# Kernel optimization log

Measured on AMD Instinct MI355X. Metric: run time of the kernel, lower is better.

Reference implementation:

```python
import jax, jax.numpy as jnp
import numpy as np

LN_EPS = 1e-5  # nn.LayerNorm default
N_HEAD = 12


def layer_norm(x, w, b, eps=LN_EPS):
    m = jnp.mean(x, axis=-1, keepdims=True)
    v = jnp.var(x, axis=-1, keepdims=True)
    return (x - m) * jax.lax.rsqrt(v + eps) * w + b


def mha(x, in_proj_w, in_proj_b, out_w, out_b, n_head):
    # x: [B,S,D]; self-attention, q=k=v=x (torch nn.MultiheadAttention math)
    B, S, D = x.shape
    hd = D // n_head
    qkv = x @ in_proj_w.T + in_proj_b              # [B,S,3D]
    q, k, v = jnp.split(qkv, 3, axis=-1)
    q = q.reshape(B, S, n_head, hd)
    k = k.reshape(B, S, n_head, hd)
    v = v.reshape(B, S, n_head, hd)
    scale = 1.0 / jnp.sqrt(jnp.asarray(hd, x.dtype))
    scores = jnp.einsum('bqhd,bkhd->bhqk', q, k) * scale  # [B,H,S,S]
    attn = jax.nn.softmax(scores, axis=-1)
    o = jnp.einsum('bhqk,bkhd->bqhd', attn, v).reshape(B, S, D)
    return o @ out_w.T + out_b


def setup_inputs() -> dict:
    key = jax.random.key(0)
    ks = jax.random.split(key, 8)
    B, S, D = 4, 2048, 768
    d_ff = 4 * D
    sd = 0.02
    return {
        'x': jax.random.normal(ks[0], (B, S, D), jnp.float32),
        'ln1_w': jnp.ones((D,), jnp.float32),
        'ln1_b': jnp.zeros((D,), jnp.float32),
        'in_proj_w': jax.random.normal(ks[1], (3 * D, D), jnp.float32) * sd,
        'in_proj_b': jax.random.normal(ks[2], (3 * D,), jnp.float32) * sd,
        'out_w': jax.random.normal(ks[3], (D, D), jnp.float32) * sd,
        'out_b': jax.random.normal(ks[4], (D,), jnp.float32) * sd,
        'ln2_w': jnp.ones((D,), jnp.float32),
        'ln2_b': jnp.zeros((D,), jnp.float32),
        'fc_w': jax.random.normal(ks[5], (d_ff, D), jnp.float32) * sd,
        'fc_b': jnp.zeros((d_ff,), jnp.float32),
        'proj_w': jax.random.normal(ks[6], (D, d_ff), jnp.float32) * sd,
        'proj_b': jnp.zeros((D,), jnp.float32),
    }


def reference(x, ln1_w, ln1_b, in_proj_w, in_proj_b, out_w, out_b,
              ln2_w, ln2_b, fc_w, fc_b, proj_w, proj_b):
    h = layer_norm(x, ln1_w, ln1_b)
    x = x + mha(h, in_proj_w, in_proj_b, out_w, out_b, N_HEAD)
    h2 = layer_norm(x, ln2_w, ln2_b)
    mlp = jax.nn.gelu(h2 @ fc_w.T + fc_b, approximate=False) @ proj_w.T + proj_b
    return x + mlp
```

## Files before the change

### kernel.cpp

```cpp
#include <hip/hip_runtime.h>
#include <hip/hip_bf16.h>
#include <math.h>

#define D_MODEL 768
#define N_HEADS 12
#define HD 64
#define SEQ 2048
#define BATCH 4
#define M_ROWS 8192
#define D_FF 3072
#define QKV_DIM 2304
#define LN_EPS 1e-5f
#define Q_SCALE 0.18033688011112042f

typedef __attribute__((ext_vector_type(8))) short bf16x8;
typedef __attribute__((ext_vector_type(4))) float f32x4;
typedef __hip_bfloat16 bf16;

__device__ __forceinline__ void store_val(float* p, float v) { *p = v; }
__device__ __forceinline__ void store_val(bf16* p, float v) { *p = __float2bfloat16(v); }

__device__ __forceinline__ unsigned int pack_bf16_pair(float a, float b) {
    unsigned int ua = __builtin_bit_cast(unsigned int, a) + 0x8000u;
    unsigned int ub = __builtin_bit_cast(unsigned int, b) + 0x8000u;
    return __builtin_amdgcn_perm(ub, ua, 0x07060302u);
}

__device__ __forceinline__ void async_load16(const void* g, void* l) {
    __builtin_amdgcn_global_load_lds(
        (const __attribute__((address_space(1))) void*)g,
        (__attribute__((address_space(3))) void*)l, 16, 0, 0);
}

__global__ __launch_bounds__(256) void ln1_cast(
        const float* __restrict__ x, const float* __restrict__ w,
        const float* __restrict__ b, bf16* __restrict__ y,
        const float* __restrict__ s0, bf16* __restrict__ d0, int n0,
        const float* __restrict__ s1, bf16* __restrict__ d1, int n1,
        const float* __restrict__ s2, bf16* __restrict__ d2, int n2,
        const float* __restrict__ s3, bf16* __restrict__ d3, int n3) {
    int t = threadIdx.x;
    if (blockIdx.x >= M_ROWS) {
        int i = (blockIdx.x - M_ROWS) * 256 + t;
        const float* s; bf16* d; int local = i;
        if (local < n0) { s = s0; d = d0; }
        else {
            local -= n0;
            if (local < n1) { s = s1; d = d1; }
            else {
                local -= n1;
                if (local < n2) { s = s2; d = d2; }
                else {
                    local -= n2;
                    if (local >= n3) return;
                    s = s3; d = d3;
                }
            }
        }
        float4 v = ((const float4*)s)[local];
        uint2 pk;
        pk.x = pack_bf16_pair(v.x, v.y);
        pk.y = pack_bf16_pair(v.z, v.w);
        *(uint2*)(d + local * 4) = pk;
        return;
    }
    int row = blockIdx.x;
    const float* xr = x + (size_t)row * D_MODEL;
    bf16* yr = y + (size_t)row * D_MODEL;
    float v0 = xr[t], v1 = xr[t + 256], v2 = xr[t + 512];
    float s  = v0 + v1 + v2;
    float sq = v0 * v0 + v1 * v1 + v2 * v2;
    #pragma unroll
    for (int off = 32; off; off >>= 1) {
        s  += __shfl_xor(s, off);
        sq += __shfl_xor(sq, off);
    }
    __shared__ float ss[4], ssq[4];
    int wave = t >> 6;
    if ((t & 63) == 0) { ss[wave] = s; ssq[wave] = sq; }
    __syncthreads();
    s  = ss[0] + ss[1] + ss[2] + ss[3];
    sq = ssq[0] + ssq[1] + ssq[2] + ssq[3];
    float mean = s * (1.0f / D_MODEL);
    float var  = sq * (1.0f / D_MODEL) - mean * mean;
    float rstd = rsqrtf(var + LN_EPS);
    yr[t]       = __float2bfloat16((v0 - mean) * rstd * w[t]       + b[t]);
    yr[t + 256] = __float2bfloat16((v1 - mean) * rstd * w[t + 256] + b[t + 256]);
    yr[t + 512] = __float2bfloat16((v2 - mean) * rstd * w[t + 512] + b[t + 512]);
}

template <typename OutT>
__global__ __launch_bounds__(256) void ln_kernel(const float* __restrict__ x,
                                                 const float* __restrict__ w,
                                                 const float* __restrict__ b,
                                                 OutT* __restrict__ y) {
    int row = blockIdx.x;
    const float* xr = x + (size_t)row * D_MODEL;
    OutT* yr = y + (size_t)row * D_MODEL;
    int t = threadIdx.x;
    float v0 = xr[t], v1 = xr[t + 256], v2 = xr[t + 512];
    float s  = v0 + v1 + v2;
    float sq = v0 * v0 + v1 * v1 + v2 * v2;
    #pragma unroll
    for (int off = 32; off; off >>= 1) {
        s  += __shfl_xor(s, off);
        sq += __shfl_xor(sq, off);
    }
    __shared__ float ss[4], ssq[4];
    int wave = t >> 6;
    if ((t & 63) == 0) { ss[wave] = s; ssq[wave] = sq; }
    __syncthreads();
    s  = ss[0] + ss[1] + ss[2] + ss[3];
    sq = ssq[0] + ssq[1] + ssq[2] + ssq[3];
    float mean = s * (1.0f / D_MODEL);
    float var  = sq * (1.0f / D_MODEL) - mean * mean;
    float rstd = rsqrtf(var + LN_EPS);
    store_val(yr + t,       (v0 - mean) * rstd * w[t]       + b[t]);
    store_val(yr + t + 256, (v1 - mean) * rstd * w[t + 256] + b[t + 256]);
    store_val(yr + t + 512, (v2 - mean) * rstd * w[t + 512] + b[t + 512]);
}

__device__ __forceinline__ float gelu_fast(float v) {
    float u = v * (0.7978845608f + 0.0356774081f * v * v);
    u = fminf(fmaxf(u, -10.0f), 10.0f);
    float e = __builtin_amdgcn_exp2f(u * 2.8853900818f);
    float th = (e - 1.0f) * __builtin_amdgcn_rcpf(e + 1.0f);
    return 0.5f * v * (1.0f + th);
}

template <int FUSE, typename OutT>
__global__ __launch_bounds__(256) void gemm_mfma(const bf16* __restrict__ A,
                                                 const bf16* __restrict__ W,
                                                 const float* __restrict__ bias,
                                                 const float* __restrict__ resid,
                                                 OutT* __restrict__ C,
                                                 int M, int N, int K) {
    const int BK = 64;
    __shared__ __align__(16) bf16 As[2][128 * BK];
    __shared__ __align__(16) bf16 Bs[2][128 * BK];
    int t = threadIdx.x;
    int wave = t >> 6, lane = t & 63;

    int nbx = gridDim.x;
    int w0 = blockIdx.x + nbx * blockIdx.y;
    int cpx = (nbx * gridDim.y) >> 3;
    int wg = (w0 & 7) * cpx + (w0 >> 3);
    int m_base = (wg / nbx) * 128, n_base = (wg % nbx) * 128;

    int wm = (wave >> 1) * 64, wn = (wave & 1) * 64;
    int c = lane & 15, rr = lane >> 4;
    int cx = c & 7;

    f32x4 acc[4][4] = {};

    const bf16* Ag[4]; const bf16* Bg[4];
    int loff[4];
    #pragma unroll
    for (int r = 0; r < 4; r++) {
        int s = r * 256 + t;
        int row = s >> 3, p = s & 7;
        int kc = p ^ (row & 7);
        Ag[r] = A + (size_t)(m_base + row) * K + kc * 8;
        Bg[r] = W + (size_t)(n_base + row) * K + kc * 8;
        loff[r] = (r * 256 + wave * 64) * 8;
    }

    auto STAGE = [&](int kt, int buf) {
        int k0 = kt * BK;
        #pragma unroll
        for (int r = 0; r < 4; r++) {
            async_load16(Ag[r] + k0, As[buf] + loff[r]);
            async_load16(Bg[r] + k0, Bs[buf] + loff[r]);
        }
    };

    int nk = K / BK;
    STAGE(0, 0);
    STAGE(1, 1);

    for (int ki = 0; ki < nk; ki++) {
        int cur = ki & 1;
        if (ki < nk - 1) {
            asm volatile("s_waitcnt vmcnt(8)" ::: "memory");
        } else {
            asm volatile("s_waitcnt vmcnt(0)" ::: "memory");
        }
        __builtin_amdgcn_s_barrier();
        __builtin_amdgcn_sched_barrier(0);

        bf16x8 af[2][4], bfr[2][4];
        #pragma unroll
        for (int kk = 0; kk < 2; kk++) {
            int sw = ((kk * 4 + rr) ^ cx) * 8;
            #pragma unroll
            for (int mi = 0; mi < 4; mi++)
                af[kk][mi] = *(const bf16x8*)&As[cur][(wm + mi * 16 + c) * BK + sw];
            #pragma unroll
            for (int ni = 0; ni < 4; ni++)
                bfr[kk][ni] = *(const bf16x8*)&Bs[cur][(wn + ni * 16 + c) * BK + sw];
        }
        asm volatile("s_waitcnt lgkmcnt(0)" ::: "memory");
        __builtin_amdgcn_s_barrier();
        __builtin_amdgcn_sched_barrier(0);

        if (ki + 2 < nk) STAGE(ki + 2, cur);

        __builtin_amdgcn_s_setprio(1);
        #pragma unroll
        for (int kk = 0; kk < 2; kk++)
            #pragma unroll
            for (int mi = 0; mi < 4; mi++)
                #pragma unroll
                for (int ni = 0; ni < 4; ni++)
                    acc[mi][ni] = __builtin_amdgcn_mfma_f32_16x16x32_bf16(
                        bfr[kk][ni], af[kk][mi], acc[mi][ni], 0, 0, 0);
        __builtin_amdgcn_s_setprio(0);
    }

    #pragma unroll
    for (int mi = 0; mi < 4; mi++) {
        int m = m_base + wm + mi * 16 + c;
        #pragma unroll
        for (int ni = 0; ni < 4; ni++) {
            int n0 = n_base + wn + ni * 16 + rr * 4;
            float4 bv = *(const float4*)&bias[n0];
            float v0 = acc[mi][ni][0] + bv.x;
            float v1 = acc[mi][ni][1] + bv.y;
            float v2 = acc[mi][ni][2] + bv.z;
            float v3 = acc[mi][ni][3] + bv.w;
            if (FUSE == 1) {
                v0 = gelu_fast(v0); v1 = gelu_fast(v1);
                v2 = gelu_fast(v2); v3 = gelu_fast(v3);
            }
            if (FUSE == 2) {
                float4 rv = *(const float4*)&resid[(size_t)m * N + n0];
                v0 += rv.x; v1 += rv.y; v2 += rv.z; v3 += rv.w;
            }
            if (FUSE == 3 && n0 < 768) {
                v0 *= Q_SCALE; v1 *= Q_SCALE; v2 *= Q_SCALE; v3 *= Q_SCALE;
            }
            OutT* dst = C + (size_t)m * N + n0;
            if (sizeof(OutT) == 4) {
                float4 st = {v0, v1, v2, v3};
                *(float4*)dst = st;
            } else {
                uint2 pk;
                pk.x = pack_bf16_pair(v0, v1);
                pk.y = pack_bf16_pair(v2, v3);
                *(uint2*)dst = pk;
            }
        }
    }
}

__global__ __launch_bounds__(256) void vtrans(const bf16* __restrict__ qkvb,
                                              bf16* __restrict__ vt) {
    __shared__ bf16 T[64 * 72];
    int t = threadIdx.x;
    int s0 = blockIdx.x * 64, h = blockIdx.y, b = blockIdx.z;
    const bf16* src = qkvb + (size_t)(b * SEQ) * QKV_DIM + 2 * D_MODEL + h * HD;
    #pragma unroll
    for (int i = 0; i < 2; i++) {
        int idx = i * 256 + t;
        int sr = idx >> 3, ch = idx & 7;
        uint4 v = *(const uint4*)(src + (size_t)(s0 + sr) * QKV_DIM + ch * 8);
        *(uint4*)&T[sr * 72 + ch * 8] = v;
    }
    __syncthreads();
    int dr = t >> 2, part = t & 3;
    unsigned int w[8];
    #pragma unroll
    for (int i = 0; i < 8; i++) {
        unsigned short a, bsh;
        __builtin_memcpy(&a,   &T[(part * 16 + 2 * i    ) * 72 + dr], 2);
        __builtin_memcpy(&bsh, &T[(part * 16 + 2 * i + 1) * 72 + dr], 2);
        w[i] = (unsigned int)a | ((unsigned int)bsh << 16);
    }
    bf16* dst = vt + ((size_t)((b * N_HEADS + h) * HD + dr)) * SEQ + s0 + part * 16;
    uint4 p0; p0.x = w[0]; p0.y = w[1]; p0.z = w[2]; p0.w = w[3];
    uint4 p1; p1.x = w[4]; p1.y = w[5]; p1.z = w[6]; p1.w = w[7];
    *(uint4*)dst = p0;
    *(uint4*)(dst + 8) = p1;
}

__global__ __launch_bounds__(256) void attn_mfma(const bf16* __restrict__ qkvb,
                                                 const bf16* __restrict__ vt,
                                                 bf16* __restrict__ o) {
    __shared__ __align__(16) bf16 Ks[2 * 64 * 64];
    __shared__ __align__(16) bf16 Vts[2 * 64 * 64];
    __shared__ __align__(16) bf16 Ps[128 * 64];

    int t = threadIdx.x;
    int wave = t >> 6, lane = t & 63;

    int w0 = blockIdx.x + 16 * (blockIdx.y + 12 * blockIdx.z);
    int wg = (w0 & 7) * 96 + (w0 >> 3);
    int qt = wg & 15;
    int hb = wg >> 4;
    int h = hb % 12, b = hb / 12;

    int s0 = qt * 128;
    int wq = wave * 32;
    int c = lane & 15, rr = lane >> 4;
    int cx = c & 7;

    const bf16* qbase  = qkvb + (size_t)b * SEQ * QKV_DIM + h * HD;
    const bf16* kbase  = qbase + D_MODEL;
    const bf16* vtbase = vt + (size_t)((b * N_HEADS + h) * HD) * SEQ;

    #pragma unroll
    for (int r = 0; r < 4; r++) {
        int lin = r * 256 + t;
        int qq = lin >> 3, p = lin & 7;
        int kc = p ^ (qq & 7);
        async_load16(qbase + (size_t)(s0 + qq) * QKV_DIM + kc * 8,
                     Ps + (size_t)(r * 256 + wave * 64) * 8);
    }
    #pragma unroll
    for (int r = 0; r < 2; r++) {
        int row = (r * 256 + t) >> 3;
        int kc = ((r * 256 + t) & 7) ^ (row & 7);
        async_load16(kbase + (size_t)row * QKV_DIM + kc * 8,
                     Ks + (size_t)(r * 256 + wave * 64) * 8);
        async_load16(vtbase + (size_t)row * SEQ + kc * 8,
                     Vts + (size_t)(r * 256 + wave * 64) * 8);
    }
    __syncthreads();

    bf16x8 bq[2][2];
    #pragma unroll
    for (int m = 0; m < 2; m++)
        #pragma unroll
        for (int kk = 0; kk < 2; kk++)
            bq[m][kk] = *(const bf16x8*)&Ps[(wq + m * 16 + c) * 64 + ((kk * 4 + rr) ^ cx) * 8];

    bf16x8 ones;
    #pragma unroll
    for (int i = 0; i < 8; i++) ones[i] = (short)0x3F80;

    f32x4 Oa[2][4] = {};
    f32x4 La[2] = {};

    for (int jt = 0; jt < SEQ; jt += 64) {
        int cur = (jt >> 6) & 1;
        bf16* Kb  = Ks  + cur * 4096;
        bf16* Vtb = Vts + cur * 4096;

        if (jt + 64 < SEQ) {
            bf16* Kn  = Ks  + (cur ^ 1) * 4096;
            bf16* Vtn = Vts + (cur ^ 1) * 4096;
            #pragma unroll
            for (int r = 0; r < 2; r++) {
                int row = (r * 256 + t) >> 3;
                int kc = ((r * 256 + t) & 7) ^ (row & 7);
                async_load16(kbase + (size_t)(jt + 64 + row) * QKV_DIM + kc * 8,
                             Kn + (size_t)(r * 256 + wave * 64) * 8);
                async_load16(vtbase + (size_t)row * SEQ + (jt + 64) + kc * 8,
                             Vtn + (size_t)(r * 256 + wave * 64) * 8);
            }
        }

        f32x4 St[4][2] = {};
        __builtin_amdgcn_s_setprio(1);
        #pragma unroll
        for (int kk = 0; kk < 2; kk++) {
            bf16x8 ak[4];
            #pragma unroll
            for (int jj = 0; jj < 4; jj++)
                ak[jj] = *(const bf16x8*)&Kb[(jj * 16 + c) * 64 + ((kk * 4 + rr) ^ cx) * 8];
            #pragma unroll
            for (int jj = 0; jj < 4; jj++)
                #pragma unroll
                for (int m = 0; m < 2; m++)
                    St[jj][m] = __builtin_amdgcn_mfma_f32_16x16x32_bf16(
                        ak[jj], bq[m][kk], St[jj][m], 0, 0, 0);
        }
        __builtin_amdgcn_s_setprio(0);

        #pragma unroll
        for (int jj = 0; jj < 4; jj++) {
            int off = ((jj * 2 + (rr >> 1)) ^ cx) * 8 + (rr & 1) * 4;
            #pragma unroll
            for (int m = 0; m < 2; m++) {
                float p0 = __builtin_amdgcn_exp2f(St[jj][m][0]);
                float p1 = __builtin_amdgcn_exp2f(St[jj][m][1]);
                float p2 = __builtin_amdgcn_exp2f(St[jj][m][2]);
                float p3 = __builtin_amdgcn_exp2f(St[jj][m][3]);
                uint2 pk;
                pk.x = pack_bf16_pair(p0, p1);
                pk.y = pack_bf16_pair(p2, p3);
                *(uint2*)&Ps[(wq + m * 16 + c) * 64 + off] = pk;
            }
        }

        __builtin_amdgcn_s_setprio(1);
        #pragma unroll
        for (int kk = 0; kk < 2; kk++) {
            bf16x8 ap[2];
            #pragma unroll
            for (int m = 0; m < 2; m++)
                ap[m] = *(const bf16x8*)&Ps[(wq + m * 16 + c) * 64 + ((kk * 4 + rr) ^ cx) * 8];
            #pragma unroll
            for (int m = 0; m < 2; m++)
                La[m] = __builtin_amdgcn_mfma_f32_16x16x32_bf16(
                    ap[m], ones, La[m], 0, 0, 0);
            #pragma unroll
            for (int n = 0; n < 4; n++) {
                bf16x8 bv = *(const bf16x8*)&Vtb[(n * 16 + c) * 64 + ((kk * 4 + rr) ^ cx) * 8];
                #pragma unroll
                for (int m = 0; m < 2; m++)
                    Oa[m][n] = __builtin_amdgcn_mfma_f32_16x16x32_bf16(
                        ap[m], bv, Oa[m][n], 0, 0, 0);
            }
        }
        __builtin_amdgcn_s_setprio(0);

        __syncthreads();
    }

    #pragma unroll
    for (int m = 0; m < 2; m++)
        #pragma unroll
        for (int rg = 0; rg < 4; rg++) {
            float inv = __builtin_amdgcn_rcpf(La[m][rg]);
            int q = s0 + wq + m * 16 + rr * 4 + rg;
            bf16* op = o + (size_t)(b * SEQ + q) * D_MODEL + h * HD;
            #pragma unroll
            for (int n = 0; n < 4; n++)
                op[n * 16 + c] = __float2bfloat16(Oa[m][n][rg] * inv);
        }
}

extern "C" void kernel_launch(void* const* d_in, const int* in_sizes, int n_in,
                              void* d_out, int out_size, void* d_ws, size_t ws_size,
                              hipStream_t stream) {
    const float* x         = (const float*)d_in[0];
    const float* ln1_w     = (const float*)d_in[1];
    const float* ln1_b     = (const float*)d_in[2];
    const float* in_proj_w = (const float*)d_in[3];
    const float* in_proj_b = (const float*)d_in[4];
    const float* out_w     = (const float*)d_in[5];
    const float* out_b     = (const float*)d_in[6];
    const float* ln2_w     = (const float*)d_in[7];
    const float* ln2_b     = (const float*)d_in[8];
    const float* fc_w      = (const float*)d_in[9];
    const float* fc_b      = (const float*)d_in[10];
    const float* proj_w    = (const float*)d_in[11];
    const float* proj_b    = (const float*)d_in[12];

    float* out = (float*)d_out;
    char*  ws  = (char*)d_ws;

    bf16* qkvb = (bf16*)ws;
    bf16* vt   = (bf16*)(ws + 37748736);
    bf16* ff   = (bf16*)ws;
    bf16* h    = (bf16*)(ws + 50331648);
    bf16* o    = (bf16*)(ws + 62914560);
    bf16* wbf  = (bf16*)(ws + 75497472);
    bf16* wqkv_b  = wbf;
    bf16* wout_b  = wqkv_b + (size_t)QKV_DIM * D_MODEL;
    bf16* wfc_b   = wout_b + (size_t)D_MODEL * D_MODEL;
    bf16* wproj_b = wfc_b  + (size_t)D_FF * D_MODEL;

    int n0 = QKV_DIM * D_MODEL / 4, n1 = D_MODEL * D_MODEL / 4;
    int n2 = D_FF * D_MODEL / 4,    n3 = D_MODEL * D_FF / 4;
    int cast_blocks = (n0 + n1 + n2 + n3 + 255) / 256;

    ln1_cast<<<M_ROWS + cast_blocks, 256, 0, stream>>>(
        x, ln1_w, ln1_b, h,
        in_proj_w, wqkv_b, n0, out_w, wout_b, n1, fc_w, wfc_b, n2, proj_w, wproj_b, n3);
    gemm_mfma<3, bf16><<<dim3(QKV_DIM / 128, M_ROWS / 128), 256, 0, stream>>>(
        h, wqkv_b, in_proj_b, nullptr, qkvb, M_ROWS, QKV_DIM, D_MODEL);
    vtrans<<<dim3(SEQ / 64, N_HEADS, BATCH), 256, 0, stream>>>(qkvb, vt);
    attn_mfma<<<dim3(SEQ / 128, N_HEADS, BATCH), 256, 0, stream>>>(qkvb, vt, o);
    gemm_mfma<2, float><<<dim3(D_MODEL / 128, M_ROWS / 128), 256, 0, stream>>>(
        o, wout_b, out_b, x, out, M_ROWS, D_MODEL, D_MODEL);
    ln_kernel<bf16><<<M_ROWS, 256, 0, stream>>>(out, ln2_w, ln2_b, h);
    gemm_mfma<1, bf16><<<dim3(D_FF / 128, M_ROWS / 128), 256, 0, stream>>>(
        h, wfc_b, fc_b, nullptr, ff, M_ROWS, D_FF, D_MODEL);
    gemm_mfma<2, float><<<dim3(D_MODEL / 128, M_ROWS / 128), 256, 0, stream>>>(
        ff, wproj_b, proj_b, out, out, M_ROWS, D_MODEL, D_FF);
}
```

Measured before the change: 382.8 us.

## Add 256x256-tile 8-wave GEMM with ping-pong MFMA scheduling for QKV and FC

Adds a new GEMM kernel that uses 256x256 output tiles, 512 threads, double-buffered async LDS loads and a four-phase interleave of LDS fragment reads with MFMA blocks under s_setprio. It replaces the 128x128 GEMM for the QKV projection and the FC+GELU projection. The larger tiles raise arithmetic intensity and cut global and LDS traffic per FLOP. In exchange they use 128 KB of LDS per block, a heavy accumulator register load and fewer blocks, which can hurt occupancy and tail balance (QKV gets 288 blocks, FC 384).

Result: slower. 394.4 us (+3.0%).

```diff
diff --git a/kernel.cpp b/kernel.cpp
--- a/kernel.cpp
+++ b/kernel.cpp
@@ -129,6 +129,182 @@
 }
 
 template <int FUSE, typename OutT>
+__global__ __launch_bounds__(512, 2) void gemm_256(const bf16* __restrict__ A,
+                                                   const bf16* __restrict__ W,
+                                                   const float* __restrict__ bias,
+                                                   OutT* __restrict__ C,
+                                                   int M, int N, int K) {
+    __shared__ __align__(16) bf16 As[2][256 * 64];
+    __shared__ __align__(16) bf16 Bs[2][256 * 64];
+    int t = threadIdx.x;
+    int wave = t >> 6, lane = t & 63;
+
+    int nbx = gridDim.x;
+    int w0 = blockIdx.x + nbx * blockIdx.y;
+    int cpx = (nbx * gridDim.y) >> 3;
+    int wg = (w0 & 7) * cpx + (w0 >> 3);
+    int m_base = (wg / nbx) * 256, n_base = (wg % nbx) * 256;
+
+    int wm = (wave >> 2) * 128;
+    int wn = (wave & 3) * 64;
+    int c = lane & 15, rr = lane >> 4;
+    int cx = c & 7;
+
+    f32x4 acc[8][4] = {};
+
+    const bf16* Ag[4]; const bf16* Bg[4];
+    int loff[4];
+    #pragma unroll
+    for (int r = 0; r < 4; r++) {
+        int s = r * 512 + t;
+        int row = s >> 3, p = s & 7;
+        int kc = p ^ (row & 7);
+        Ag[r] = A + (size_t)(m_base + row) * K + kc * 8;
+        Bg[r] = W + (size_t)(n_base + row) * K + kc * 8;
+        loff[r] = (r * 512 + wave * 64) * 8;
+    }
+
+    auto STAGE = [&](int kt, int buf) {
+        int k0 = kt * 64;
+        #pragma unroll
+        for (int r = 0; r < 4; r++) {
+            async_load16(Ag[r] + k0, As[buf] + loff[r]);
+            async_load16(Bg[r] + k0, Bs[buf] + loff[r]);
+        }
+    };
+
+    int nk = K / 64;
+    STAGE(0, 0);
+    STAGE(1, 1);
+
+    for (int ki = 0; ki < nk; ki++) {
+        int cur = ki & 1;
+        const bf16* Ab = As[cur];
+        const bf16* Bb = Bs[cur];
+
+        if (ki < nk - 1) {
+            asm volatile("s_waitcnt vmcnt(8)" ::: "memory");
+        } else {
+            asm volatile("s_waitcnt vmcnt(0)" ::: "memory");
+        }
+        __builtin_amdgcn_s_barrier();
+        __builtin_amdgcn_sched_barrier(0);
+
+        bf16x8 af[4][2];
+        bf16x8 bfr[2][2][2];
+
+        #pragma unroll
+        for (int mi = 0; mi < 4; mi++)
+            #pragma unroll
+            for (int kk = 0; kk < 2; kk++)
+                af[mi][kk] = *(const bf16x8*)&Ab[(wm + mi * 16 + c) * 64 + (((kk << 2) + rr) ^ cx) * 8];
+        #pragma unroll
+        for (int ni = 0; ni < 2; ni++)
+            #pragma unroll
+            for (int kk = 0; kk < 2; kk++)
+                bfr[0][ni][kk] = *(const bf16x8*)&Bb[(wn + ni * 16 + c) * 64 + (((kk << 2) + rr) ^ cx) * 8];
+        __builtin_amdgcn_s_barrier();
+        asm volatile("s_waitcnt lgkmcnt(0)" ::: "memory");
+        __builtin_amdgcn_sched_barrier(0);
+        __builtin_amdgcn_s_setprio(1);
+        #pragma unroll
+        for (int kk = 0; kk < 2; kk++)
+            #pragma unroll
+            for (int mi = 0; mi < 4; mi++)
+                #pragma unroll
+                for (int ni = 0; ni < 2; ni++)
+                    acc[mi][ni] = __builtin_amdgcn_mfma_f32_16x16x32_bf16(
+                        bfr[0][ni][kk], af[mi][kk], acc[mi][ni], 0, 0, 0);
+        __builtin_amdgcn_s_setprio(0);
+        __builtin_amdgcn_s_barrier();
+
+        #pragma unroll
+        for (int ni = 0; ni < 2; ni++)
+            #pragma unroll
+            for (int kk = 0; kk < 2; kk++)
+                bfr[1][ni][kk] = *(const bf16x8*)&Bb[(wn + 32 + ni * 16 + c) * 64 + (((kk << 2) + rr) ^ cx) * 8];
+        __builtin_amdgcn_s_barrier();
+        asm volatile("s_waitcnt lgkmcnt(0)" ::: "memory");
+        __builtin_amdgcn_sched_barrier(0);
+        __builtin_amdgcn_s_setprio(1);
+        #pragma unroll
+        for (int kk = 0; kk < 2; kk++)
+            #pragma unroll
+            for (int mi = 0; mi < 4; mi++)
+                #pragma unroll
+                for (int ni = 0; ni < 2; ni++)
+                    acc[mi][2 + ni] = __builtin_amdgcn_mfma_f32_16x16x32_bf16(
+                        bfr[1][ni][kk], af[mi][kk], acc[mi][2 + ni], 0, 0, 0);
+        __builtin_amdgcn_s_setprio(0);
+        __builtin_amdgcn_s_barrier();
+
+        #pragma unroll
+        for (int mi = 0; mi < 4; mi++)
+            #pragma unroll
+            for (int kk = 0; kk < 2; kk++)
+                af[mi][kk] = *(const bf16x8*)&Ab[(wm + 64 + mi * 16 + c) * 64 + (((kk << 2) + rr) ^ cx) * 8];
+        __builtin_amdgcn_s_barrier();
+        asm volatile("s_waitcnt lgkmcnt(0)" ::: "memory");
+        __builtin_amdgcn_sched_barrier(0);
+        __builtin_amdgcn_s_setprio(1);
+        #pragma unroll
+        for (int kk = 0; kk < 2; kk++)
+            #pragma unroll
+            for (int mi = 0; mi < 4; mi++)
+                #pragma unroll
+                for (int ni = 0; ni < 2; ni++)
+                    acc[4 + mi][2 + ni] = __builtin_amdgcn_mfma_f32_16x16x32_bf16(
+                        bfr[1][ni][kk], af[mi][kk], acc[4 + mi][2 + ni], 0, 0, 0);
+        __builtin_amdgcn_s_setprio(0);
+        __builtin_amdgcn_s_barrier();
+
+        if (ki + 2 < nk) STAGE(ki + 2, cur);
+        __builtin_amdgcn_s_setprio(1);
+        #pragma unroll
+        for (int kk = 0; kk < 2; kk++)
+            #pragma unroll
+            for (int mi = 0; mi < 4; mi++)
+                #pragma unroll
+                for (int ni = 0; ni < 2; ni++)
+                    acc[4 + mi][ni] = __builtin_amdgcn_mfma_f32_16x16x32_bf16(
+                        bfr[0][ni][kk], af[mi][kk], acc[4 + mi][ni], 0, 0, 0);
+        __builtin_amdgcn_s_setprio(0);
+        __builtin_amdgcn_s_barrier();
+    }
+
+    #pragma unroll
+    for (int mi = 0; mi < 8; mi++) {
+        int m = m_base + wm + mi * 16 + c;
+        #pragma unroll
+        for (int ni = 0; ni < 4; ni++) {
+            int n0 = n_base + wn + ni * 16 + rr * 4;
+            float4 bv = *(const float4*)&bias[n0];
+            float v0 = acc[mi][ni][0] + bv.x;
+            float v1 = acc[mi][ni][1] + bv.y;
+            float v2 = acc[mi][ni][2] + bv.z;
+            float v3 = acc[mi][ni][3] + bv.w;
+            if (FUSE == 1) {
+                v0 = gelu_fast(v0); v1 = gelu_fast(v1);
+                v2 = gelu_fast(v2); v3 = gelu_fast(v3);
+            }
+            if (FUSE == 3 && n0 < 768) {
+                v0 *= Q_SCALE; v1 *= Q_SCALE; v2 *= Q_SCALE; v3 *= Q_SCALE;
+            }
+            OutT* dst = C + (size_t)m * N + n0;
+            if (sizeof(OutT) == 4) {
+                float4 st = {v0, v1, v2, v3};
+                *(float4*)dst = st;
+            } else {
+                uint2 pk;
+                pk.x = pack_bf16_pair(v0, v1);
+                pk.y = pack_bf16_pair(v2, v3);
+                *(uint2*)dst = pk;
+            }
+        }
+    }
+}
+
+template <int FUSE, typename OutT>
 __global__ __launch_bounds__(256) void gemm_mfma(const bf16* __restrict__ A,
                                                  const bf16* __restrict__ W,
                                                  const float* __restrict__ bias,
@@ -469,15 +645,15 @@
     ln1_cast<<<M_ROWS + cast_blocks, 256, 0, stream>>>(
         x, ln1_w, ln1_b, h,
         in_proj_w, wqkv_b, n0, out_w, wout_b, n1, fc_w, wfc_b, n2, proj_w, wproj_b, n3);
-    gemm_mfma<3, bf16><<<dim3(QKV_DIM / 128, M_ROWS / 128), 256, 0, stream>>>(
-        h, wqkv_b, in_proj_b, nullptr, qkvb, M_ROWS, QKV_DIM, D_MODEL);
+    gemm_256<3, bf16><<<dim3(QKV_DIM / 256, M_ROWS / 256), 512, 0, stream>>>(
+        h, wqkv_b, in_proj_b, qkvb, M_ROWS, QKV_DIM, D_MODEL);
     vtrans<<<dim3(SEQ / 64, N_HEADS, BATCH), 256, 0, stream>>>(qkvb, vt);
     attn_mfma<<<dim3(SEQ / 128, N_HEADS, BATCH), 256, 0, stream>>>(qkvb, vt, o);
     gemm_mfma<2, float><<<dim3(D_MODEL / 128, M_ROWS / 128), 256, 0, stream>>>(
         o, wout_b, out_b, x, out, M_ROWS, D_MODEL, D_MODEL);
     ln_kernel<bf16><<<M_ROWS, 256, 0, stream>>>(out, ln2_w, ln2_b, h);
-    gemm_mfma<1, bf16><<<dim3(D_FF / 128, M_ROWS / 128), 256, 0, stream>>>(
-        h, wfc_b, fc_b, nullptr, ff, M_ROWS, D_FF, D_MODEL);
+    gemm_256<1, bf16><<<dim3(D_FF / 256, M_ROWS / 256), 512, 0, stream>>>(
+        h, wfc_b, fc_b, ff, M_ROWS, D_FF, D_MODEL);
     gemm_mfma<2, float><<<dim3(D_MODEL / 128, M_ROWS / 128), 256, 0, stream>>>(
         ff, wproj_b, proj_b, out, out, M_ROWS, D_MODEL, D_FF);
 }
```
